# Optimization experiments

Measured on AMD Instinct MI355X. Metric: run time of the kernel, lower is better.

The kernel has to match this reference:

```python
import jax, jax.numpy as jnp
import numpy as np

P_DROP = 0.5  # prenet dropout rate (applied even at inference, per original code)


def _dropout(x, key):
    keep = jax.random.bernoulli(key, 1.0 - P_DROP, x.shape)
    return jnp.where(keep, x / (1.0 - P_DROP), 0.0)


def _lstm_cell(x, h, c, Wx, Wh, b):
    z = x @ Wx + h @ Wh + b                      # [B, 4R]
    i, f, g, o = jnp.split(z, 4, axis=-1)        # keras gate order i,f,c,o
    c_new = jax.nn.sigmoid(f) * c + jax.nn.sigmoid(i) * jnp.tanh(g)
    h_new = jax.nn.sigmoid(o) * jnp.tanh(c_new)
    return h_new, c_new


def setup_inputs() -> dict:
    key = jax.random.key(0)
    ks = jax.random.split(key, 24)
    B, T, V, M = 128, 512, 512, 80
    A, R, PRE = 128, 1024, 256
    OUT = M * 1 + 1  # mel_dim * step_reduction + 1 (stop token)
    sc = lambda k, shape: (jax.random.normal(k, shape) * 0.05).astype(jnp.float32)
    return {
        'encodings': jax.random.normal(ks[0], (B, T, V), jnp.float32),
        'mels': jax.random.normal(ks[1], (B, M), jnp.float32),
        'prev_align': jnp.zeros((B, T), jnp.float32).at[:, 0].set(1.0),
        'h1': jnp.zeros((B, R), jnp.float32),
        'c1': jnp.zeros((B, R), jnp.float32),
        'h2': jnp.zeros((B, R), jnp.float32),
        'c2': jnp.zeros((B, R), jnp.float32),
        'W_pre1': sc(ks[2], (M, PRE)), 'b_pre1': jnp.zeros((PRE,), jnp.float32),
        'W_pre2': sc(ks[3], (PRE, PRE)), 'b_pre2': jnp.zeros((PRE,), jnp.float32),
        'W_q': sc(ks[4], (PRE, A)), 'W_k': sc(ks[5], (V, A)),
        'b_k': jnp.zeros((A,), jnp.float32), 'v_a': sc(ks[6], (A,)),
        'b_score': jnp.zeros((), jnp.float32),
        'Wx1': sc(ks[7], (PRE + V, 4 * R)), 'Wh1': sc(ks[8], (R, 4 * R)),
        'b_l1': jnp.zeros((4 * R,), jnp.float32),
        'Wx2': sc(ks[9], (R, 4 * R)), 'Wh2': sc(ks[10], (R, 4 * R)),
        'b_l2': jnp.zeros((4 * R,), jnp.float32),
        'W_proj': sc(ks[11], (R + V, OUT)), 'b_proj': jnp.zeros((OUT,), jnp.float32),
    }


def reference(encodings, mels, prev_align, h1, c1, h2, c2,
              W_pre1, b_pre1, W_pre2, b_pre2,
              W_q, W_k, b_k, v_a, b_score,
              Wx1, Wh1, b_l1, Wx2, Wh2, b_l2,
              W_proj, b_proj):
    # --- Prenet: Dense->ReLU->Dropout x2 (dropout always on, fixed key for determinism)
    dk1, dk2 = jax.random.split(jax.random.key(7))
    x = _dropout(jax.nn.relu(mels @ W_pre1 + b_pre1), dk1)
    x = _dropout(jax.nn.relu(x @ W_pre2 + b_pre2), dk2)          # [B, 256]

    # --- Bahdanau monotonic attention (parallel recurrence, Raffel et al.)
    q = x @ W_q                                                  # [B, A]
    k = encodings @ W_k + b_k                                    # [B, T, A]
    score = jnp.einsum('bta,a->bt', jnp.tanh(q[:, None, :] + k), v_a) + b_score
    p = jax.nn.sigmoid(score)                                    # [B, T] choose probs
    one_m_p = 1.0 - p
    cp_excl = jnp.concatenate(
        [jnp.ones_like(p[:, :1]), jnp.cumprod(one_m_p, axis=1)[:, :-1]], axis=1)
    alignments = p * cp_excl * jnp.cumsum(
        prev_align / jnp.clip(cp_excl, 1e-10, 1.0), axis=1)      # [B, T]
    attentions = jnp.einsum('bt,btv->bv', alignments, encodings) # [B, V]

    # --- Stacked LSTM cells
    rnn_in = jnp.concatenate([x, attentions], axis=-1)           # [B, 256+512]
    h1n, c1n = _lstm_cell(rnn_in, h1, c1, Wx1, Wh1, b_l1)
    h2n, c2n = _lstm_cell(h1n, h2, c2, Wx2, Wh2, b_l2)

    # --- Projection + split mel / stop
    proj_in = jnp.concatenate([h2n, attentions], axis=-1)        # [B, 1024+512]
    proj = proj_in @ W_proj + b_proj                             # [B, 81]
    mel_out, stops = proj[:, :-1], proj[:, -1:]
    return (mel_out, stops, alignments, (h1n, c1n, h2n, c2n))
```

## Files before the change

### kernel.cpp

```cpp
#include <hip/hip_runtime.h>
#include <math.h>

typedef float f32x4 __attribute__((ext_vector_type(4)));
typedef __bf16 bf16x8 __attribute__((ext_vector_type(8)));
typedef __bf16 bf16x4 __attribute__((ext_vector_type(4)));

struct u2 { unsigned a, b; };

__host__ __device__ constexpr u2 threefry_ce(unsigned k0, unsigned k1,
                                             unsigned c0, unsigned c1) {
  unsigned ks2 = k0 ^ k1 ^ 0x1BD11BDAu;
  unsigned x0 = c0 + k0, x1 = c1 + k1;
#define ROTL(v, n) (((v) << (n)) | ((v) >> (32 - (n))))
#define R4(a, b, c, d)                                   \
  { x0 += x1; x1 = ROTL(x1, a); x1 ^= x0;                \
    x0 += x1; x1 = ROTL(x1, b); x1 ^= x0;                \
    x0 += x1; x1 = ROTL(x1, c); x1 ^= x0;                \
    x0 += x1; x1 = ROTL(x1, d); x1 ^= x0; }
  R4(13, 15, 26, 6);  x0 += k1;  x1 += ks2 + 1u;
  R4(17, 29, 16, 24); x0 += ks2; x1 += k0 + 2u;
  R4(13, 15, 26, 6);  x0 += k0;  x1 += k1 + 3u;
  R4(17, 29, 16, 24); x0 += k1;  x1 += ks2 + 4u;
  R4(13, 15, 26, 6);  x0 += ks2; x1 += k0 + 5u;
  return u2{x0, x1};
#undef R4
#undef ROTL
}

constexpr u2 DK0 = threefry_ce(0u, 7u, 0u, 0u);
constexpr u2 DK1 = threefry_ce(0u, 7u, 0u, 1u);

__device__ __forceinline__ float dropout_scale(int layer, unsigned i) {
  unsigned k0 = layer ? DK1.a : DK0.a;
  unsigned k1 = layer ? DK1.b : DK0.b;
  unsigned ks2 = k0 ^ k1 ^ 0x1BD11BDAu;
  unsigned x0 = 0u + k0, x1 = i + k1;
#define ROTL(v, n) (((v) << (n)) | ((v) >> (32 - (n))))
#define R4(a, b, c, d)                                   \
  { x0 += x1; x1 = ROTL(x1, a); x1 ^= x0;                \
    x0 += x1; x1 = ROTL(x1, b); x1 ^= x0;                \
    x0 += x1; x1 = ROTL(x1, c); x1 ^= x0;                \
    x0 += x1; x1 = ROTL(x1, d); x1 ^= x0; }
  R4(13, 15, 26, 6);  x0 += k1;  x1 += ks2 + 1u;
  R4(17, 29, 16, 24); x0 += ks2; x1 += k0 + 2u;
  R4(13, 15, 26, 6);  x0 += k0;  x1 += k1 + 3u;
  R4(17, 29, 16, 24); x0 += k1;  x1 += ks2 + 4u;
  R4(13, 15, 26, 6);  x0 += ks2; x1 += k0 + 5u;
#undef R4
#undef ROTL
  unsigned bits = x0 ^ x1;
  return (bits & 0x80000000u) ? 0.0f : 2.0f;
}

__device__ __forceinline__ float sigmoidf(float x) {
  return 1.0f / (1.0f + expf(-x));
}

#define CP_CUTOFF 64
#define CP_THRESH 1e-13f

__global__ __launch_bounds__(256) void prenet_kernel(
    const float* __restrict__ mels, const float* __restrict__ W1,
    const float* __restrict__ b1, const float* __restrict__ W2,
    const float* __restrict__ b2, const float* __restrict__ Wq,
    const float* __restrict__ Wk, __bf16* __restrict__ WkT,
    const float* __restrict__ h1, __bf16* __restrict__ h1bf,
    const float* __restrict__ h2, __bf16* __restrict__ h2bf,
    float* __restrict__ rnn_in, float* __restrict__ q_out) {
  int blk = blockIdx.x;
  int j = threadIdx.x;
  if (blk >= 256) {
    int base = (blk - 256) * 2048 + j * 8;
    float4 v0 = *reinterpret_cast<const float4*>(&h2[base]);
    float4 v1 = *reinterpret_cast<const float4*>(&h2[base + 4]);
    bf16x8 w;
    w[0] = (__bf16)v0.x; w[1] = (__bf16)v0.y; w[2] = (__bf16)v0.z; w[3] = (__bf16)v0.w;
    w[4] = (__bf16)v1.x; w[5] = (__bf16)v1.y; w[6] = (__bf16)v1.z; w[7] = (__bf16)v1.w;
    *reinterpret_cast<bf16x8*>(&h2bf[base]) = w;
    return;
  }
  if (blk >= 192) {
    int base = (blk - 192) * 2048 + j * 8;
    float4 v0 = *reinterpret_cast<const float4*>(&h1[base]);
    float4 v1 = *reinterpret_cast<const float4*>(&h1[base + 4]);
    bf16x8 w;
    w[0] = (__bf16)v0.x; w[1] = (__bf16)v0.y; w[2] = (__bf16)v0.z; w[3] = (__bf16)v0.w;
    w[4] = (__bf16)v1.x; w[5] = (__bf16)v1.y; w[6] = (__bf16)v1.z; w[7] = (__bf16)v1.w;
    *reinterpret_cast<bf16x8*>(&h1bf[base]) = w;
    return;
  }
  if (blk >= 128) {
    int gid = (blk - 128) * 256 + j;
    int a = gid & 127;
    int k4 = (gid >> 7) * 4;
    bf16x4 w;
    for (int i = 0; i < 4; ++i) w[i] = (__bf16)Wk[(size_t)(k4 + i) * 128 + a];
    *reinterpret_cast<bf16x4*>(&WkT[(size_t)a * 512 + k4]) = w;
    return;
  }
  int b = blk;
  __shared__ float mel_s[80];
  __shared__ float x1_s[256];
  __shared__ float x2_s[256];
  if (j < 80) mel_s[j] = mels[b * 80 + j];
  rnn_in[(size_t)b * 768 + 256 + j] = 0.0f;
  rnn_in[(size_t)b * 768 + 512 + j] = 0.0f;
  __syncthreads();
  float s = b1[j];
  for (int m = 0; m < 80; ++m) s = fmaf(mel_s[m], W1[m * 256 + j], s);
  s = fmaxf(s, 0.0f) * dropout_scale(0, (unsigned)(b * 256 + j));
  x1_s[j] = s;
  __syncthreads();
  float s2 = b2[j];
  for (int m = 0; m < 256; ++m) s2 = fmaf(x1_s[m], W2[m * 256 + j], s2);
  s2 = fmaxf(s2, 0.0f) * dropout_scale(1, (unsigned)(b * 256 + j));
  x2_s[j] = s2;
  rnn_in[(size_t)b * 768 + j] = s2;
  __syncthreads();
  if (j < 128) {
    float sq = 0.0f;
    for (int m = 0; m < 256; ++m) sq = fmaf(x2_s[m], Wq[m * 128 + j], sq);
    q_out[b * 128 + j] = sq;
  }
}

__global__ __launch_bounds__(256) void score16_kernel(
    const float* __restrict__ enc, const __bf16* __restrict__ WkT,
    const float* __restrict__ bk, const float* __restrict__ q,
    const float* __restrict__ va_g, const float* __restrict__ bscore,
    float* __restrict__ score) {
  int b = blockIdx.y;
  int t0 = blockIdx.x * 16;
  int tid = threadIdx.x;
  int lane = tid & 63, wid = tid >> 6;
  __shared__ __align__(16) __bf16 Eb[16 * 64];
  __shared__ float red[16][4];

  f32x4 acc[2];
#pragma unroll
  for (int j = 0; j < 2; ++j) acc[j] = (f32x4){0.f, 0.f, 0.f, 0.f};

  float qv[2], vav[2];
  int an[2];
#pragma unroll
  for (int j = 0; j < 2; ++j) {
    int a = wid * 32 + j * 16 + (lane & 15);
    an[j] = a;
    qv[j] = q[b * 128 + a] + bk[a];
    vav[j] = va_g[a];
  }
  int er = tid >> 4, ek4 = (tid & 15) * 4;
  int koct = (lane >> 4) * 8;
  int tl = lane & 15;

  for (int k0 = 0; k0 < 512; k0 += 64) {
    __syncthreads();
    {
      const float4 v = *reinterpret_cast<const float4*>(
          &enc[((size_t)(b * 512 + t0 + er)) * 512 + k0 + ek4]);
      bf16x4 w;
      w[0] = (__bf16)v.x; w[1] = (__bf16)v.y;
      w[2] = (__bf16)v.z; w[3] = (__bf16)v.w;
      *reinterpret_cast<bf16x4*>(&Eb[er * 64 + (ek4 ^ ((er & 7) << 3))]) = w;
    }
    __syncthreads();
#pragma unroll
    for (int kk = 0; kk < 64; kk += 32) {
      int kl = kk + koct;
      bf16x8 af = *reinterpret_cast<const bf16x8*>(
          &Eb[tl * 64 + (kl ^ ((tl & 7) << 3))]);
      bf16x8 bfr[2];
#pragma unroll
      for (int j = 0; j < 2; ++j)
        bfr[j] = *reinterpret_cast<const bf16x8*>(
            &WkT[(size_t)an[j] * 512 + k0 + kl]);
#pragma unroll
      for (int j = 0; j < 2; ++j)
        acc[j] = __builtin_amdgcn_mfma_f32_16x16x32_bf16(af, bfr[j], acc[j], 0, 0, 0);
    }
  }

#pragma unroll
  for (int r = 0; r < 4; ++r) {
    float s = tanhf(qv[0] + acc[0][r]) * vav[0] +
              tanhf(qv[1] + acc[1][r]) * vav[1];
    s += __shfl_xor(s, 1, 64);
    s += __shfl_xor(s, 2, 64);
    s += __shfl_xor(s, 4, 64);
    s += __shfl_xor(s, 8, 64);
    if ((lane & 15) == 0) red[(lane >> 4) * 4 + r][wid] = s;
  }
  __syncthreads();
  if (tid < 16)
    score[b * 512 + t0 + tid] =
        red[tid][0] + red[tid][1] + red[tid][2] + red[tid][3] + bscore[0];
}

__global__ __launch_bounds__(256) void score64_kernel(
    const float* __restrict__ enc, const __bf16* __restrict__ WkT,
    const float* __restrict__ bk, const float* __restrict__ q,
    const float* __restrict__ va_g, const float* __restrict__ bscore,
    float* __restrict__ score, int t_base) {
  int b = blockIdx.y;
  int tid = threadIdx.x;
  __shared__ float fl[64];
  if (tid < 64) fl[tid] = 1.0f - sigmoidf(score[b * 512 + tid]);
  __syncthreads();
  for (int off = 32; off >= 1; off >>= 1) {
    if (tid < off) fl[tid] *= fl[tid + off];
    __syncthreads();
  }
  if (fl[0] < CP_THRESH) return;

  int t0 = t_base + blockIdx.x * 64;
  int lane = tid & 63, wid = tid >> 6;
  int wr = wid >> 1, wc = wid & 1;
  __shared__ __align__(16) __bf16 Eb[64 * 64];
  __shared__ float red[64][2];

  f32x4 acc[2][4];
#pragma unroll
  for (int i = 0; i < 2; ++i)
#pragma unroll
    for (int j = 0; j < 4; ++j) acc[i][j] = (f32x4){0.f, 0.f, 0.f, 0.f};

  float qv[4], vav[4];
  int an[4];
#pragma unroll
  for (int j = 0; j < 4; ++j) {
    int a = wc * 64 + j * 16 + (lane & 15);
    an[j] = a;
    qv[j] = q[b * 128 + a] + bk[a];
    vav[j] = va_g[a];
  }
  int er = tid >> 4, ek4 = (tid & 15) * 4;
  int koct = (lane >> 4) * 8;

  for (int k0 = 0; k0 < 512; k0 += 64) {
    __syncthreads();
#pragma unroll
    for (int p = 0; p < 4; ++p) {
      int t = er + p * 16;
      const float4 v = *reinterpret_cast<const float4*>(
          &enc[((size_t)(b * 512 + t0 + t)) * 512 + k0 + ek4]);
      bf16x4 w;
      w[0] = (__bf16)v.x; w[1] = (__bf16)v.y;
      w[2] = (__bf16)v.z; w[3] = (__bf16)v.w;
      *reinterpret_cast<bf16x4*>(&Eb[t * 64 + (ek4 ^ ((t & 7) << 3))]) = w;
    }
    __syncthreads();
#pragma unroll
    for (int kk = 0; kk < 64; kk += 32) {
      int kl = kk + koct;
      bf16x8 af[2], bfr[4];
#pragma unroll
      for (int i = 0; i < 2; ++i) {
        int t = wr * 32 + i * 16 + (lane & 15);
        af[i] = *reinterpret_cast<const bf16x8*>(&Eb[t * 64 + (kl ^ ((t & 7) << 3))]);
      }
#pragma unroll
      for (int j = 0; j < 4; ++j)
        bfr[j] = *reinterpret_cast<const bf16x8*>(
            &WkT[(size_t)an[j] * 512 + k0 + kl]);
#pragma unroll
      for (int i = 0; i < 2; ++i)
#pragma unroll
        for (int j = 0; j < 4; ++j)
          acc[i][j] = __builtin_amdgcn_mfma_f32_16x16x32_bf16(
              af[i], bfr[j], acc[i][j], 0, 0, 0);
    }
  }

#pragma unroll
  for (int i = 0; i < 2; ++i) {
#pragma unroll
    for (int r = 0; r < 4; ++r) {
      float s = 0.0f;
#pragma unroll
      for (int j = 0; j < 4; ++j) s += tanhf(qv[j] + acc[i][j][r]) * vav[j];
      s += __shfl_xor(s, 1, 64);
      s += __shfl_xor(s, 2, 64);
      s += __shfl_xor(s, 4, 64);
      s += __shfl_xor(s, 8, 64);
      if ((lane & 15) == 0)
        red[wr * 32 + i * 16 + (lane >> 4) * 4 + r][wc] = s;
    }
  }
  __syncthreads();
  if (tid < 64)
    score[b * 512 + t0 + tid] = red[tid][0] + red[tid][1] + bscore[0];
}

__global__ __launch_bounds__(512) void scan_kernel(
    const float* __restrict__ score, const float* __restrict__ prev_align,
    float* __restrict__ align_out) {
  int b = blockIdx.x, t = threadIdx.x;
  int lane = t & 63, wv = t >> 6;
  __shared__ float wtot[8];
  __shared__ float flg_s;
  float sc0 = score[b * 512 + t];
  if (wv == 0) {
    float om = 1.0f - sigmoidf(sc0);
    for (int off = 32; off >= 1; off >>= 1) om *= __shfl_xor(om, off, 64);
    if (lane == 0) flg_s = om;
  }
  __syncthreads();
  int flg = flg_s < CP_THRESH;
  float sc = (t < CP_CUTOFF || !flg) ? sc0 : -1e30f;
  float p = sigmoidf(sc);
  float x = 1.0f - p;
#pragma unroll
  for (int off = 1; off < 64; off <<= 1) {
    float v = __shfl_up(x, off, 64);
    if (lane >= off) x *= v;
  }
  if (lane == 63) wtot[wv] = x;
  __syncthreads();
  float pre = 1.0f;
  for (int w = 0; w < wv; ++w) pre *= wtot[w];
  x *= pre;
  float xm1 = __shfl_up(x, 1, 64);
  float cp_excl = (lane == 0) ? ((wv == 0) ? 1.0f : pre) : xm1;
  float denom = fminf(fmaxf(cp_excl, 1e-10f), 1.0f);
  float r = prev_align[b * 512 + t] / denom;
  float y = r;
#pragma unroll
  for (int off = 1; off < 64; off <<= 1) {
    float v = __shfl_up(y, off, 64);
    if (lane >= off) y += v;
  }
  __syncthreads();
  if (lane == 63) wtot[wv] = y;
  __syncthreads();
  float spre = 0.0f;
  for (int w = 0; w < wv; ++w) spre += wtot[w];
  y += spre;
  align_out[b * 512 + t] = p * cp_excl * y;
}

__global__ __launch_bounds__(256) void att_part_kernel(
    const float* __restrict__ align, const float* __restrict__ enc,
    float* __restrict__ rnn_in) {
  int tc = blockIdx.x;
  int vt = blockIdx.y;
  int b = blockIdx.z;
  int tid = threadIdx.x;
  int v = vt * 256 + tid;
  __shared__ float al[64];
  __shared__ int lastnz;
  if (tid < 64) {
    float a = align[b * 512 + tc * 64 + tid];
    al[tid] = a;
    unsigned long long m = __ballot(a != 0.0f);
    if (tid == 0) lastnz = m ? (63 - __clzll(m)) : -1;
  }
  __syncthreads();
  int ln = lastnz;
  if (ln < 0) return;
  float acc = 0.0f;
  const float* encp = &enc[((size_t)(b * 512 + tc * 64)) * 512 + v];
#pragma unroll 4
  for (int tt = 0; tt <= ln; ++tt)
    acc = fmaf(al[tt], encp[(size_t)tt * 512], acc);
  atomicAdd(&rnn_in[(size_t)b * 768 + 256 + v], acc);
}

__global__ __launch_bounds__(256) void zgemm_mfma_kernel(
    const float* __restrict__ A0, const __bf16* __restrict__ Abf0, int K0,
    const float* __restrict__ W0,
    const float* __restrict__ A1, const __bf16* __restrict__ Abf1, int K1,
    const float* __restrict__ W1,
    float* __restrict__ parts) {
  int cb = blockIdx.x;
  int zp = blockIdx.y;
  int seg = zp >> 1, kh = zp & 1;
  const float* A = seg ? A1 : A0;
  const __bf16* Abf = seg ? Abf1 : Abf0;
  const float* W = seg ? W1 : W0;
  int K = seg ? K1 : K0;
  int kc = K >> 1;
  int kbeg = kh * kc, kend = kbeg + kc;
  int tid = threadIdx.x;
  int lane = tid & 63, wid = tid >> 6;
  int wr = wid >> 1, wc = wid & 1;
  __shared__ __align__(16) __bf16 Ab[128 * 64];

  f32x4 acc[4];
#pragma unroll
  for (int i = 0; i < 4; ++i) acc[i] = (f32x4){0.f, 0.f, 0.f, 0.f};

  int n_base = cb * 32 + wc * 16 + (lane & 15);
  int koct = (lane >> 4) * 8;

  for (int k0 = kbeg; k0 < kend; k0 += 64) {
    __syncthreads();
    if (Abf) {
      int r4 = tid >> 3;
      int k8 = (tid & 7) * 8;
#pragma unroll
      for (int p = 0; p < 4; ++p) {
        int row = r4 + p * 32;
        bf16x8 v = *reinterpret_cast<const bf16x8*>(
            &Abf[(size_t)row * K + k0 + k8]);
        *reinterpret_cast<bf16x8*>(&Ab[row * 64 + (k8 ^ ((row & 7) << 3))]) = v;
      }
    } else {
      int r = tid >> 4;
      int k4 = (tid & 15) * 4;
#pragma unroll
      for (int p = 0; p < 8; ++p) {
        int row = r + p * 16;
        const float4 v = *reinterpret_cast<const float4*>(
            &A[(size_t)row * K + k0 + k4]);
        bf16x4 w;
        w[0] = (__bf16)v.x; w[1] = (__bf16)v.y;
        w[2] = (__bf16)v.z; w[3] = (__bf16)v.w;
        *reinterpret_cast<bf16x4*>(&Ab[row * 64 + (k4 ^ ((row & 7) << 3))]) = w;
      }
    }
    __syncthreads();
#pragma unroll
    for (int kk = 0; kk < 64; kk += 32) {
      const float* wq = W + (size_t)(k0 + kk + koct) * 4096 + n_base;
      bf16x8 bfr;
#pragma unroll
      for (int j = 0; j < 8; ++j) bfr[j] = (__bf16)wq[(size_t)j * 4096];
      int kl = kk + koct;
#pragma unroll
      for (int i = 0; i < 4; ++i) {
        int t = wr * 64 + i * 16 + (lane & 15);
        bf16x8 af = *reinterpret_cast<const bf16x8*>(
            &Ab[t * 64 + (kl ^ ((t & 7) << 3))]);
        acc[i] = __builtin_amdgcn_mfma_f32_16x16x32_bf16(af, bfr, acc[i], 0, 0, 0);
      }
    }
  }

  float* outp = parts + (size_t)zp * (128 * 4096);
#pragma unroll
  for (int i = 0; i < 4; ++i)
#pragma unroll
    for (int r = 0; r < 4; ++r) {
      int row = wr * 64 + i * 16 + ((lane >> 4) << 2) + r;
      int col = cb * 32 + wc * 16 + (lane & 15);
      outp[(size_t)row * 4096 + col] = acc[i][r];
    }
}

__global__ __launch_bounds__(256) void gate_kernel(
    const float* __restrict__ parts, const float* __restrict__ bias,
    const float* __restrict__ c_prev, float* __restrict__ h_out,
    float* __restrict__ c_out, __bf16* __restrict__ h_bf) {
  int idx = blockIdx.x * 256 + threadIdx.x;
  int b = idx >> 10, j = idx & 1023;
  float zv[4];
  for (int g = 0; g < 4; ++g) {
    size_t off = (size_t)b * 4096 + g * 1024 + j;
    float s = bias[g * 1024 + j];
    for (int p = 0; p < 4; ++p) s += parts[(size_t)p * (128 * 4096) + off];
    zv[g] = s;
  }
  float ig = sigmoidf(zv[0]);
  float fg = sigmoidf(zv[1]);
  float gg = tanhf(zv[2]);
  float og = sigmoidf(zv[3]);
  float cn = fg * c_prev[idx] + ig * gg;
  float hn = og * tanhf(cn);
  h_out[idx] = hn;
  c_out[idx] = cn;
  h_bf[idx] = (__bf16)hn;
}

__global__ __launch_bounds__(1024) void gateproj_kernel(
    const float* __restrict__ parts, const float* __restrict__ bias,
    const float* __restrict__ c_prev, const float* __restrict__ rnn_in,
    const float* __restrict__ Wp, const float* __restrict__ bp,
    float* __restrict__ h_out, float* __restrict__ c_out,
    float* __restrict__ mel, float* __restrict__ stops) {
  int b = blockIdx.x;
  int j = threadIdx.x;
  __shared__ float row[1536];
  __shared__ float red[12][81];
  int idx = b * 1024 + j;
  float zv[4];
#pragma unroll
  for (int g = 0; g < 4; ++g) {
    size_t off = (size_t)b * 4096 + g * 1024 + j;
    float s = bias[g * 1024 + j];
#pragma unroll
    for (int p = 0; p < 4; ++p) s += parts[(size_t)p * (128 * 4096) + off];
    zv[g] = s;
  }
  float ig = sigmoidf(zv[0]);
  float fg = sigmoidf(zv[1]);
  float gg = tanhf(zv[2]);
  float og = sigmoidf(zv[3]);
  float cn = fg * c_prev[idx] + ig * gg;
  float hn = og * tanhf(cn);
  h_out[idx] = hn;
  c_out[idx] = cn;
  row[j] = hn;
  if (j < 512) row[1024 + j] = rnn_in[(size_t)b * 768 + 256 + j];
  __syncthreads();
  if (j < 972) {
    int o = j % 81, part = j / 81;
    int m0 = part * 128;
    float s = 0.0f;
    for (int m = m0; m < m0 + 128; ++m) s = fmaf(row[m], Wp[m * 81 + o], s);
    red[part][o] = s;
  }
  __syncthreads();
  if (j < 81) {
    float s = bp[j];
#pragma unroll
    for (int p = 0; p < 12; ++p) s += red[p][j];
    if (j < 80) mel[b * 80 + j] = s;
    else stops[b] = s;
  }
}

extern "C" void kernel_launch(void* const* d_in, const int* in_sizes, int n_in,
                              void* d_out, int out_size, void* d_ws,
                              size_t ws_size, hipStream_t stream) {
  const float* enc  = (const float*)d_in[0];
  const float* mels = (const float*)d_in[1];
  const float* prev = (const float*)d_in[2];
  const float* h1   = (const float*)d_in[3];
  const float* c1   = (const float*)d_in[4];
  const float* h2   = (const float*)d_in[5];
  const float* c2   = (const float*)d_in[6];
  const float* Wp1  = (const float*)d_in[7];
  const float* bp1  = (const float*)d_in[8];
  const float* Wp2  = (const float*)d_in[9];
  const float* bp2  = (const float*)d_in[10];
  const float* Wq   = (const float*)d_in[11];
  const float* Wk   = (const float*)d_in[12];
  const float* bk   = (const float*)d_in[13];
  const float* va   = (const float*)d_in[14];
  const float* bsc  = (const float*)d_in[15];
  const float* Wx1  = (const float*)d_in[16];
  const float* Wh1  = (const float*)d_in[17];
  const float* bl1  = (const float*)d_in[18];
  const float* Wx2  = (const float*)d_in[19];
  const float* Wh2  = (const float*)d_in[20];
  const float* bl2  = (const float*)d_in[21];
  const float* Wpj  = (const float*)d_in[22];
  const float* bpj  = (const float*)d_in[23];

  float* out = (float*)d_out;
  float* mel    = out;
  float* stops  = out + 10240;
  float* aligno = out + 10368;
  float* h1n    = out + 75904;
  float* c1n    = out + 206976;
  float* h2n    = out + 338048;
  float* c2n    = out + 469120;

  float* ws = (float*)d_ws;
  float* q_ws   = ws;
  float* sc_ws  = ws + 16384;
  float* rnn_in = ws + 81920;
  float* parts  = ws + 180224;
  __bf16* h1bf  = (__bf16*)(ws + 2277376);
  __bf16* h2bf  = (__bf16*)(ws + 2342912);
  __bf16* h1nbf = (__bf16*)(ws + 2408448);
  __bf16* WkT = (__bf16*)parts;

  hipLaunchKernelGGL(prenet_kernel, dim3(320), dim3(256), 0, stream,
                     mels, Wp1, bp1, Wp2, bp2, Wq, Wk, WkT,
                     h1, h1bf, h2, h2bf, rnn_in, q_ws);
  hipLaunchKernelGGL(score16_kernel, dim3(4, 128), dim3(256), 0, stream,
                     enc, WkT, bk, q_ws, va, bsc, sc_ws);
  hipLaunchKernelGGL(score64_kernel, dim3(7, 128), dim3(256), 0, stream,
                     enc, WkT, bk, q_ws, va, bsc, sc_ws, 64);
  hipLaunchKernelGGL(scan_kernel, dim3(128), dim3(512), 0, stream,
                     sc_ws, prev, aligno);
  hipLaunchKernelGGL(att_part_kernel, dim3(8, 2, 128), dim3(256), 0, stream,
                     aligno, enc, rnn_in);
  hipLaunchKernelGGL(zgemm_mfma_kernel, dim3(128, 4), dim3(256), 0, stream,
                     rnn_in, (const __bf16*)nullptr, 768, Wx1,
                     h1, h1bf, 1024, Wh1, parts);
  hipLaunchKernelGGL(gate_kernel, dim3(512), dim3(256), 0, stream,
                     parts, bl1, c1, h1n, c1n, h1nbf);
  hipLaunchKernelGGL(zgemm_mfma_kernel, dim3(128, 4), dim3(256), 0, stream,
                     h1n, h1nbf, 1024, Wx2,
                     h2, h2bf, 1024, Wh2, parts);
  hipLaunchKernelGGL(gateproj_kernel, dim3(128), dim3(1024), 0, stream,
                     parts, bl2, c2, rnn_in, Wpj, bpj, h2n, c2n, mel, stops);
}
```

Baseline: 90.18 us.

## Drop split-K in LSTM GEMM, vectorize attention and gate kernels

```diff
diff --git a/kernel.cpp b/kernel.cpp
--- a/kernel.cpp
+++ b/kernel.cpp
@@ -342,12 +342,13 @@
     const float* __restrict__ align, const float* __restrict__ enc,
     float* __restrict__ rnn_in) {
   int tc = blockIdx.x;
-  int vt = blockIdx.y;
-  int b = blockIdx.z;
+  int b = blockIdx.y;
   int tid = threadIdx.x;
-  int v = vt * 256 + tid;
+  int th = tid >> 7;
+  int vs = tid & 127;
   __shared__ float al[64];
   __shared__ int lastnz;
+  __shared__ f32x4 part0[128];
   if (tid < 64) {
     float a = align[b * 512 + tc * 64 + tid];
     al[tid] = a;
@@ -357,12 +358,30 @@
   __syncthreads();
   int ln = lastnz;
   if (ln < 0) return;
-  float acc = 0.0f;
-  const float* encp = &enc[((size_t)(b * 512 + tc * 64)) * 512 + v];
+  f32x4 acc = (f32x4){0.f, 0.f, 0.f, 0.f};
+  int tbeg = th * 32;
+  int tend = min(ln + 1, tbeg + 32);
+  const f32x4* ep = reinterpret_cast<const f32x4*>(enc) +
+                    ((size_t)(b * 512 + tc * 64) * 128) + vs;
 #pragma unroll 4
-  for (int tt = 0; tt <= ln; ++tt)
-    acc = fmaf(al[tt], encp[(size_t)tt * 512], acc);
-  atomicAdd(&rnn_in[(size_t)b * 768 + 256 + v], acc);
+  for (int tt = tbeg; tt < tend; ++tt) {
+    float a = al[tt];
+    f32x4 e = ep[(size_t)tt * 128];
+    acc.x = fmaf(a, e.x, acc.x);
+    acc.y = fmaf(a, e.y, acc.y);
+    acc.z = fmaf(a, e.z, acc.z);
+    acc.w = fmaf(a, e.w, acc.w);
+  }
+  if (th == 0) part0[vs] = acc;
+  __syncthreads();
+  if (th == 1) {
+    f32x4 p0 = part0[vs];
+    float* dst = &rnn_in[(size_t)b * 768 + 256 + vs * 4];
+    atomicAdd(&dst[0], acc.x + p0.x);
+    atomicAdd(&dst[1], acc.y + p0.y);
+    atomicAdd(&dst[2], acc.z + p0.z);
+    atomicAdd(&dst[3], acc.w + p0.w);
+  }
 }
 
 __global__ __launch_bounds__(256) void zgemm_mfma_kernel(
@@ -372,27 +391,23 @@
     const float* __restrict__ W1,
     float* __restrict__ parts) {
   int cb = blockIdx.x;
-  int zp = blockIdx.y;
-  int seg = zp >> 1, kh = zp & 1;
+  int seg = blockIdx.y;
   const float* A = seg ? A1 : A0;
   const __bf16* Abf = seg ? Abf1 : Abf0;
   const float* W = seg ? W1 : W0;
   int K = seg ? K1 : K0;
-  int kc = K >> 1;
-  int kbeg = kh * kc, kend = kbeg + kc;
   int tid = threadIdx.x;
-  int lane = tid & 63, wid = tid >> 6;
-  int wr = wid >> 1, wc = wid & 1;
+  int lane = tid & 63, wr = tid >> 6;
   __shared__ __align__(16) __bf16 Ab[128 * 64];
 
-  f32x4 acc[4];
-#pragma unroll
-  for (int i = 0; i < 4; ++i) acc[i] = (f32x4){0.f, 0.f, 0.f, 0.f};
-
-  int n_base = cb * 32 + wc * 16 + (lane & 15);
+  f32x4 acc[2];
+#pragma unroll
+  for (int i = 0; i < 2; ++i) acc[i] = (f32x4){0.f, 0.f, 0.f, 0.f};
+
+  int n_base = cb * 16 + (lane & 15);
   int koct = (lane >> 4) * 8;
 
-  for (int k0 = kbeg; k0 < kend; k0 += 64) {
+  for (int k0 = 0; k0 < K; k0 += 64) {
     __syncthreads();
     if (Abf) {
       int r4 = tid >> 3;
@@ -427,8 +442,8 @@
       for (int j = 0; j < 8; ++j) bfr[j] = (__bf16)wq[(size_t)j * 4096];
       int kl = kk + koct;
 #pragma unroll
-      for (int i = 0; i < 4; ++i) {
-        int t = wr * 64 + i * 16 + (lane & 15);
+      for (int i = 0; i < 2; ++i) {
+        int t = wr * 32 + i * 16 + (lane & 15);
         bf16x8 af = *reinterpret_cast<const bf16x8*>(
             &Ab[t * 64 + (kl ^ ((t & 7) << 3))]);
         acc[i] = __builtin_amdgcn_mfma_f32_16x16x32_bf16(af, bfr, acc[i], 0, 0, 0);
@@ -436,13 +451,13 @@
     }
   }
 
-  float* outp = parts + (size_t)zp * (128 * 4096);
-#pragma unroll
-  for (int i = 0; i < 4; ++i)
+  float* outp = parts + (size_t)seg * (128 * 4096);
+#pragma unroll
+  for (int i = 0; i < 2; ++i)
 #pragma unroll
     for (int r = 0; r < 4; ++r) {
-      int row = wr * 64 + i * 16 + ((lane >> 4) << 2) + r;
-      int col = cb * 32 + wc * 16 + (lane & 15);
+      int row = wr * 32 + i * 16 + ((lane >> 4) << 2) + r;
+      int col = cb * 16 + (lane & 15);
       outp[(size_t)row * 4096 + col] = acc[i][r];
     }
 }
@@ -451,24 +466,34 @@
     const float* __restrict__ parts, const float* __restrict__ bias,
     const float* __restrict__ c_prev, float* __restrict__ h_out,
     float* __restrict__ c_out, __bf16* __restrict__ h_bf) {
-  int idx = blockIdx.x * 256 + threadIdx.x;
-  int b = idx >> 10, j = idx & 1023;
-  float zv[4];
+  int b = blockIdx.x;
+  int j4 = threadIdx.x * 4;
+  f32x4 zv[4];
+#pragma unroll
   for (int g = 0; g < 4; ++g) {
-    size_t off = (size_t)b * 4096 + g * 1024 + j;
-    float s = bias[g * 1024 + j];
-    for (int p = 0; p < 4; ++p) s += parts[(size_t)p * (128 * 4096) + off];
+    size_t off = (size_t)b * 4096 + g * 1024 + j4;
+    f32x4 s = *reinterpret_cast<const f32x4*>(&bias[g * 1024 + j4]);
+    s += *reinterpret_cast<const f32x4*>(&parts[off]);
+    s += *reinterpret_cast<const f32x4*>(&parts[(size_t)(128 * 4096) + off]);
     zv[g] = s;
   }
-  float ig = sigmoidf(zv[0]);
-  float fg = sigmoidf(zv[1]);
-  float gg = tanhf(zv[2]);
-  float og = sigmoidf(zv[3]);
-  float cn = fg * c_prev[idx] + ig * gg;
-  float hn = og * tanhf(cn);
-  h_out[idx] = hn;
-  c_out[idx] = cn;
-  h_bf[idx] = (__bf16)hn;
+  int idx = b * 1024 + j4;
+  f32x4 cp = *reinterpret_cast<const f32x4*>(&c_prev[idx]);
+  f32x4 hn, cn;
+  bf16x4 hb;
+#pragma unroll
+  for (int c = 0; c < 4; ++c) {
+    float ig = sigmoidf(zv[0][c]);
+    float fg = sigmoidf(zv[1][c]);
+    float gg = tanhf(zv[2][c]);
+    float og = sigmoidf(zv[3][c]);
+    float cc = fg * cp[c] + ig * gg;
+    float hh = og * tanhf(cc);
+    cn[c] = cc; hn[c] = hh; hb[c] = (__bf16)hh;
+  }
+  *reinterpret_cast<f32x4*>(&h_out[idx]) = hn;
+  *reinterpret_cast<f32x4*>(&c_out[idx]) = cn;
+  *reinterpret_cast<bf16x4*>(&h_bf[idx]) = hb;
 }
 
 __global__ __launch_bounds__(1024) void gateproj_kernel(
@@ -488,7 +513,7 @@
     size_t off = (size_t)b * 4096 + g * 1024 + j;
     float s = bias[g * 1024 + j];
 #pragma unroll
-    for (int p = 0; p < 4; ++p) s += parts[(size_t)p * (128 * 4096) + off];
+    for (int p = 0; p < 2; ++p) s += parts[(size_t)p * (128 * 4096) + off];
     zv[g] = s;
   }
   float ig = sigmoidf(zv[0]);
@@ -575,14 +600,14 @@
                      enc, WkT, bk, q_ws, va, bsc, sc_ws, 64);
   hipLaunchKernelGGL(scan_kernel, dim3(128), dim3(512), 0, stream,
                      sc_ws, prev, aligno);
-  hipLaunchKernelGGL(att_part_kernel, dim3(8, 2, 128), dim3(256), 0, stream,
+  hipLaunchKernelGGL(att_part_kernel, dim3(8, 128), dim3(256), 0, stream,
                      aligno, enc, rnn_in);
-  hipLaunchKernelGGL(zgemm_mfma_kernel, dim3(128, 4), dim3(256), 0, stream,
+  hipLaunchKernelGGL(zgemm_mfma_kernel, dim3(256, 2), dim3(256), 0, stream,
                      rnn_in, (const __bf16*)nullptr, 768, Wx1,
                      h1, h1bf, 1024, Wh1, parts);
-  hipLaunchKernelGGL(gate_kernel, dim3(512), dim3(256), 0, stream,
+  hipLaunchKernelGGL(gate_kernel, dim3(128), dim3(256), 0, stream,
                      parts, bl1, c1, h1n, c1n, h1nbf);
-  hipLaunchKernelGGL(zgemm_mfma_kernel, dim3(128, 4), dim3(256), 0, stream,
+  hipLaunchKernelGGL(zgemm_mfma_kernel, dim3(256, 2), dim3(256), 0, stream,
                      h1n, h1nbf, 1024, Wx2,
                      h2, h2bf, 1024, Wh2, parts);
   hipLaunchKernelGGL(gateproj_kernel, dim3(128), dim3(1024), 0, stream,
```

Measured after the change: 106.7 us. 1.18x slower.
